# Kernel tuning notes

Measured on AMD Instinct MI355X. Metric: run time of the kernel, lower is better.

## Reference

```python
import jax, jax.numpy as jnp
import numpy as np

CUTOFFS = [0, 19997, 39997, 199997, 267735]  # cutoff_ends
SIZES = [19997, 20000, 160000, 67738]
DEMBS = [1024, 256, 64, 16]  # d_embed // div_val**i, div_val=4
N, D_PROJ = 1024, 1024


def setup_inputs() -> dict:
    key = jax.random.key(0)
    ks = jax.random.split(key, 20)
    inp = {
        "hidden": jax.random.normal(ks[0], (N, D_PROJ), jnp.float32),
        "target": jax.random.randint(ks[1], (N,), 0, CUTOFFS[-1], dtype=jnp.int64),
    }
    for i in range(4):
        inp[f"W{i}"] = 0.02 * jax.random.normal(ks[2 + 3 * i], (SIZES[i], DEMBS[i]), jnp.float32)
        inp[f"b{i}"] = jnp.zeros((SIZES[i],), jnp.float32)
        inp[f"p{i}"] = 0.02 * jax.random.normal(ks[3 + 3 * i], (D_PROJ, DEMBS[i]), jnp.float32)
    inp["cluster_weight"] = 0.02 * jax.random.normal(ks[14], (3, DEMBS[0]), jnp.float32)
    inp["cluster_bias"] = jnp.zeros((3,), jnp.float32)
    return inp


def _logit(hidden, W, b, p):
    # einsum('bd,de,ev->bv', hidden, proj, weight.T) + bias
    return (hidden @ p) @ W.T + b


def reference(hidden, target, W0, b0, p0, W1, b1, p1, W2, b2, p2, W3, b3, p3,
              cluster_weight, cluster_bias):
    n = hidden.shape[0]
    rows = jnp.arange(n)
    shortlist = W0.shape[0]  # 19997

    # head cluster: shortlist vocab + 3 cluster logits
    head_w = jnp.concatenate([W0, cluster_weight], axis=0)   # [shortlist+3, d_embed]
    head_b = jnp.concatenate([b0, cluster_bias], axis=0)
    head_lp = jax.nn.log_softmax(_logit(hidden, head_w, head_b, p0), axis=-1)  # [N, shortlist+3]

    masks = [target < CUTOFFS[1]]
    lps = [head_lp[rows, jnp.clip(target, 0, shortlist - 1)]]

    for i, (W, b, p) in enumerate([(W1, b1, p1), (W2, b2, p2), (W3, b3, p3)], start=1):
        l_idx, r_idx = CUTOFFS[i], CUTOFFS[i + 1]
        tail_lp = jax.nn.log_softmax(_logit(hidden, W, b, p), axis=-1)  # [N, r-l]
        rel = jnp.clip(target - l_idx, 0, r_idx - l_idx - 1)
        lps.append(head_lp[:, shortlist + i - 1] + tail_lp[rows, rel])
        masks.append((target >= l_idx) & (target < r_idx))

    logprob = jnp.select(masks, lps)
    return -logprob  # nll, shape [N]
```

## Files before the change

### kernel.cpp

```cpp
#include <hip/hip_runtime.h>
#include <stdint.h>

typedef short v8s __attribute__((ext_vector_type(8)));
typedef float f4 __attribute__((ext_vector_type(4)));
typedef unsigned short u16;
typedef unsigned int u32;

#define CUT1 19997
#define CUT2 39997
#define CUT3 199997
#define NROWS 1024
#define LDP 1360

#define NG_HEAD 157
#define NG_T1 40
#define NG_T2 157
#define NG_T3 67

__device__ __forceinline__ u32 pack2(float a, float b) {
    return (__float_as_uint(a) >> 16) | (__float_as_uint(b) & 0xffff0000u);
}
__device__ __forceinline__ float b2f(u16 h) { return __uint_as_float(((u32)h) << 16); }
__device__ __forceinline__ u16 f2b(float f) { return (u16)(__float_as_uint(f) >> 16); }

__device__ __forceinline__ void gload16(const void* g, void* l) {
    __builtin_amdgcn_global_load_lds(
        (const __attribute__((address_space(1))) u32*)g,
        (__attribute__((address_space(3))) u32*)l, 16, 0, 0);
}

__device__ __forceinline__ void cast8(const float* __restrict__ in, u16* __restrict__ out, size_t j) {
    const float4* p = (const float4*)(in + j * 8);
    float4 a = p[0], b = p[1];
    uint4 o = { pack2(a.x, a.y), pack2(a.z, a.w), pack2(b.x, b.y), pack2(b.z, b.w) };
    *(uint4*)(out + j * 8) = o;
}

__global__ __launch_bounds__(256) void prep_small_k(
    const float* __restrict__ hidden,
    const float* __restrict__ p0, const float* __restrict__ p1,
    const float* __restrict__ p2, const float* __restrict__ p3,
    const int* __restrict__ target,
    u16* __restrict__ hb, u16* __restrict__ pTb,
    int* __restrict__ cnt, int* __restrict__ slot,
    int* __restrict__ rowmap)
{
    int bid = blockIdx.x;
    int tid = threadIdx.x;

    if (bid < 512) {
        cast8(hidden, hb, bid * 256 + tid);
        return;
    }
    if (bid < 1888) {
        int b = bid - 512;
        const float* src; int d, rowOff, bx, by;
        if (b < 1024)      { src = p0; d = 1024; rowOff = 0;    bx = b & 31;          by = b >> 5; }
        else if (b < 1280) { src = p1; d = 256;  rowOff = 1024; bx = (b - 1024) & 7;  by = (b - 1024) >> 3; }
        else if (b < 1344) { src = p2; d = 64;   rowOff = 1280; bx = (b - 1280) & 1;  by = (b - 1280) >> 1; }
        else               { src = p3; d = 16;   rowOff = 1344; bx = 0;               by = b - 1344; }
        __shared__ float tile[32][33];
        int tx = tid & 31, ty = tid >> 5;
        int x = bx * 32 + tx;
        int ybase = by * 32;
#pragma unroll
        for (int j = 0; j < 4; ++j) {
            int r = ty + j * 8;
            tile[r][tx] = (x < d) ? src[(size_t)(ybase + r) * d + x] : 0.f;
        }
        __syncthreads();
#pragma unroll
        for (int j = 0; j < 4; ++j) {
            int x2 = bx * 32 + ty + j * 8;
            if (x2 < d) pTb[(size_t)(rowOff + x2) * 1024 + ybase + tx] = f2b(tile[tx][ty + j * 8]);
        }
        return;
    }

    __shared__ int lcnt[3];
    for (int i = tid; i < 3072; i += 256) rowmap[i] = 0;
    if (tid < 3) lcnt[tid] = 0;
    __syncthreads();
    for (int r = tid; r < NROWS; r += 256) {
        int t = target[r];
        int c = (t < CUT1) ? -1 : (t < CUT2) ? 0 : (t < CUT3) ? 1 : 2;
        int s = -1;
        if (c >= 0) {
            s = atomicAdd(&lcnt[c], 1);
            rowmap[c * 1024 + s] = r;
        }
        slot[r] = s;
    }
    __syncthreads();
    if (tid < 3) cnt[tid] = lcnt[tid];
}

template<int MODE, int NCOL>
__device__ __forceinline__ void gemm_body(
    u16* __restrict__ As, u16* __restrict__ Bs,
    const u16* __restrict__ A, int lda, const int* __restrict__ rowmap,
    const u16* __restrict__ B, int ldb,
    const float* __restrict__ bias, int N, int K,
    u16* __restrict__ Cout, int ldc,
    float* __restrict__ pout, const int* __restrict__ count,
    int bx, int byg)
{
    const int tid = threadIdx.x;
    const int rbase = bx * 128;
    if (MODE == 1 && count) {
        int c = *count;
        if (rbase >= ((c + 127) & ~127)) return;
    }

    const int wave = tid >> 6, lane = tid & 63;
    const int l4 = lane & 15, quad = lane >> 4;
    const int wg = (wave >> 1) * 4;
    const int cg = (wave & 1) * 4;

    const int g0 = tid >> 6, seg0 = (tid >> 4) & 3, r0 = tid & 15;
    const int s1 = 256 + tid;
    const int g1 = s1 >> 6, seg1 = (s1 >> 4) & 3, r1 = s1 & 15;

    const u16 *Asrc0, *Asrc1;
    {
        int ar0 = rbase + g0 * 16 + r0, ar1 = rbase + g1 * 16 + r1;
        if (rowmap) { ar0 = rowmap[ar0]; ar1 = rowmap[ar1]; }
        Asrc0 = A + (size_t)ar0 * lda + seg0 * 8;
        Asrc1 = A + (size_t)ar1 * lda + seg1 * 8;
    }
    u16* Ad0 = &As[tid * 8]; u16* Ad1 = &As[(256 + tid) * 8];
    u16* Bd0 = &Bs[tid * 8]; u16* Bd1 = &Bs[(256 + tid) * 8];

    float part[4][4];
    if (MODE == 1) {
#pragma unroll
        for (int r = 0; r < 4; ++r)
#pragma unroll
            for (int g = 0; g < 4; ++g) part[r][g] = 0.f;
    }

    const int wr = wg * 16, wc = cg * 16;

    for (int ct = 0; ct < NCOL; ++ct) {
        const int cbase = (byg * NCOL + ct) * 128;
        int bc0 = cbase + g0 * 16 + r0; if (bc0 >= N) bc0 = N - 1;
        int bc1 = cbase + g1 * 16 + r1; if (bc1 >= N) bc1 = N - 1;
        const u16* Bsrc0 = B + (size_t)bc0 * ldb + seg0 * 8;
        const u16* Bsrc1 = B + (size_t)bc1 * ldb + seg1 * 8;

        f4 acc[4][4] = {};
        for (int kk = 0; kk < K; kk += 32) {
            gload16(Asrc0 + kk, Ad0);
            gload16(Asrc1 + kk, Ad1);
            gload16(Bsrc0 + kk, Bd0);
            gload16(Bsrc1 + kk, Bd1);
            __syncthreads();
            v8s af[4], bf[4];
#pragma unroll
            for (int r = 0; r < 4; ++r)
                af[r] = *(const v8s*)&As[((wg + r) * 64 + quad * 16 + l4) * 8];
#pragma unroll
            for (int c = 0; c < 4; ++c)
                bf[c] = *(const v8s*)&Bs[((cg + c) * 64 + quad * 16 + l4) * 8];
#pragma unroll
            for (int r = 0; r < 4; ++r)
#pragma unroll
                for (int c = 0; c < 4; ++c)
                    acc[r][c] = __builtin_amdgcn_mfma_f32_16x16x32_bf16(af[r], bf[c], acc[r][c], 0, 0, 0);
            __syncthreads();
        }

        if (MODE == 0) {
#pragma unroll
            for (int c = 0; c < 4; ++c) {
                int col = cbase + wc + c * 16 + l4;
                if (col < N) {
#pragma unroll
                    for (int r = 0; r < 4; ++r)
#pragma unroll
                        for (int g = 0; g < 4; ++g) {
                            int row = rbase + wr + r * 16 + quad * 4 + g;
                            Cout[(size_t)row * ldc + col] = f2b(acc[r][c][g]);
                        }
                }
            }
        } else {
#pragma unroll
            for (int c = 0; c < 4; ++c) {
                int col = cbase + wc + c * 16 + l4;
                if (col < N) {
                    float bb = bias[col];
#pragma unroll
                    for (int r = 0; r < 4; ++r)
#pragma unroll
                        for (int g = 0; g < 4; ++g)
                            part[r][g] += __expf(acc[r][c][g] + bb);
                }
            }
        }
    }

    if (MODE == 1) {
#pragma unroll
        for (int off = 1; off < 16; off <<= 1)
#pragma unroll
            for (int r = 0; r < 4; ++r)
#pragma unroll
                for (int g = 0; g < 4; ++g)
                    part[r][g] += __shfl_xor(part[r][g], off);
        float v = part[0][0];
#pragma unroll
        for (int r = 0; r < 4; ++r)
#pragma unroll
            for (int g = 0; g < 4; ++g)
                if (l4 == r * 4 + g) v = part[r][g];
        int rowoff = (l4 >> 2) * 16 + quad * 4 + (l4 & 3);
        float* lbuf = (float*)As;
        lbuf[(wave & 1) * 128 + wr + rowoff] = v;
        __syncthreads();
        if (tid < 128) pout[rbase + tid] = lbuf[tid] + lbuf[128 + tid];
    }
}

#define CP_E0 2559616
#define CP_E1 3199616
#define CP_E2 4479616
__global__ __launch_bounds__(256) void castproj_k(
    const u16* __restrict__ hb, const u16* __restrict__ pTb, u16* __restrict__ proj,
    const float* __restrict__ W0, const float* __restrict__ W1,
    const float* __restrict__ W2, const float* __restrict__ W3,
    u16* __restrict__ W0b, u16* __restrict__ W1b,
    u16* __restrict__ W2b, u16* __restrict__ W3b)
{
    __shared__ __align__(16) u16 As[4096];
    __shared__ __align__(16) u16 Bs[4096];
    int bid = blockIdx.x;
    if (bid < 88) {
        gemm_body<0, 1>(As, Bs, hb, 1024, nullptr, pTb, 1024, nullptr, 1360, 1024,
                        proj, LDP, nullptr, nullptr, bid & 7, bid >> 3);
        return;
    }
    int i = (bid - 88) * 256 + threadIdx.x;
    if (i < CP_E0) { cast8(W0, W0b, i); return; }
    if (i < CP_E1) { cast8(W1, W1b, i - CP_E0); return; }
    if (i < CP_E2) { cast8(W2, W2b, i - CP_E1); return; }
    int r = i - CP_E2;
    if (r >= 67738) return;
    const float4* p = (const float4*)(W3 + (size_t)r * 16);
    float4 a = p[0], b = p[1], c = p[2], d = p[3];
    uint4 o0 = { pack2(a.x, a.y), pack2(a.z, a.w), pack2(b.x, b.y), pack2(b.z, b.w) };
    uint4 o1 = { pack2(c.x, c.y), pack2(c.z, c.w), pack2(d.x, d.y), pack2(d.z, d.w) };
    uint4 z = { 0, 0, 0, 0 };
    uint4* q = (uint4*)(W3b + (size_t)r * 32);
    q[0] = o0; q[1] = o1; q[2] = z; q[3] = z;
}

#define SE_GRID 3368
__global__ __launch_bounds__(256) void sumexp_k(
    const u16* __restrict__ proj,
    const u16* __restrict__ W0b, const u16* __restrict__ W1b,
    const u16* __restrict__ W2b, const u16* __restrict__ W3b,
    const float* __restrict__ b0, const float* __restrict__ b1,
    const float* __restrict__ b2, const float* __restrict__ b3,
    float* __restrict__ Ph, float* __restrict__ Pt1,
    float* __restrict__ Pt2, float* __restrict__ Pt3,
    const int* __restrict__ rmap, const int* __restrict__ cnt)
{
    __shared__ __align__(16) u16 As[4096];
    __shared__ __align__(16) u16 Bs[4096];
    int bid = blockIdx.x;
    if (bid < 1256) {
        gemm_body<1, 1>(As, Bs, proj, LDP, nullptr, W0b, 1024, b0, CUT1, 1024,
                        nullptr, 0, Ph + (size_t)(bid >> 3) * 1024, nullptr, bid & 7, bid >> 3);
    } else if (bid < 1576) {
        int rel = bid - 1256;
        gemm_body<1, 4>(As, Bs, proj + 1024, LDP, rmap, W1b, 256, b1, 20000, 256,
                        nullptr, 0, Pt1 + (size_t)(rel >> 3) * 1024, cnt + 0, rel & 7, rel >> 3);
    } else if (bid < 2832) {
        int rel = bid - 1576;
        gemm_body<1, 8>(As, Bs, proj + 1280, LDP, rmap + 1024, W2b, 64, b2, 160000, 64,
                        nullptr, 0, Pt2 + (size_t)(rel >> 3) * 1024, cnt + 1, rel & 7, rel >> 3);
    } else {
        int rel = bid - 2832;
        gemm_body<1, 8>(As, Bs, proj + 1344, LDP, rmap + 2048, W3b, 32, b3, 67738, 32,
                        nullptr, 0, Pt3 + (size_t)(rel >> 3) * 1024, cnt + 2, rel & 7, rel >> 3);
    }
}

__global__ __launch_bounds__(256) void final_k(
    const u16* __restrict__ proj, const int* __restrict__ target, const int* __restrict__ slot,
    const float* __restrict__ cw, const float* __restrict__ cb,
    const float* __restrict__ W0, const float* __restrict__ b0,
    const float* __restrict__ W1, const float* __restrict__ b1,
    const float* __restrict__ W2, const float* __restrict__ b2,
    const float* __restrict__ W3, const float* __restrict__ b3,
    const float* __restrict__ Ph, const float* __restrict__ Pt1,
    const float* __restrict__ Pt2, const float* __restrict__ Pt3,
    float* __restrict__ out)
{
    int row = blockIdx.x * 4 + (threadIdx.x >> 6);
    int lane = threadIdx.x & 63;
    const u16* pr = proj + (size_t)row * LDP;

    float c0 = 0.f, c1 = 0.f, c2 = 0.f;
    for (int k = lane; k < 1024; k += 64) {
        float pv = b2f(pr[k]);
        c0 += pv * cw[k]; c1 += pv * cw[1024 + k]; c2 += pv * cw[2048 + k];
    }
    float hs = 0.f;
    for (int g = lane; g < NG_HEAD; g += 64) hs += Ph[g * 1024 + row];

    int t = target[row];
    const float* W; const float* bb; int K, off, rel;
    const float* Pc = Ph; int gc = 0;
    if (t < CUT1)      { W = W0; bb = b0; K = 1024; off = 0;    rel = t; }
    else if (t < CUT2) { W = W1; bb = b1; K = 256;  off = 1024; rel = t - CUT1; Pc = Pt1; gc = NG_T1; }
    else if (t < CUT3) { W = W2; bb = b2; K = 64;   off = 1280; rel = t - CUT2; Pc = Pt2; gc = NG_T2; }
    else               { W = W3; bb = b3; K = 16;   off = 1344; rel = t - CUT3; Pc = Pt3; gc = NG_T3; }

    float ts = 0.f;
    int s = slot[row];
    if (s >= 0) {
        for (int g = lane; g < gc; g += 64) ts += Pc[g * 1024 + s];
    }
    float acc = 0.f;
    const float* wr = W + (size_t)rel * K;
    for (int k = lane; k < K; k += 64) acc += b2f(pr[off + k]) * wr[k];

#pragma unroll
    for (int o2 = 1; o2 < 64; o2 <<= 1) {
        c0 += __shfl_xor(c0, o2); c1 += __shfl_xor(c1, o2); c2 += __shfl_xor(c2, o2);
        hs += __shfl_xor(hs, o2); ts += __shfl_xor(ts, o2); acc += __shfl_xor(acc, o2);
    }

    if (lane == 0) {
        c0 += cb[0]; c1 += cb[1]; c2 += cb[2];
        float tl = acc + bb[rel];
        float lseh = __logf(hs + __expf(c0) + __expf(c1) + __expf(c2));
        float lp;
        if (t < CUT1) lp = tl - lseh;
        else {
            int c = (t < CUT2) ? 0 : (t < CUT3) ? 1 : 2;
            float cc = (c == 0) ? c0 : (c == 1) ? c1 : c2;
            lp = (cc - lseh) + (tl - __logf(ts));
        }
        out[row] = -lp;
    }
}

__global__ void cast_bf16_k(const float* __restrict__ in, u16* __restrict__ out, int n8) {
    int i = blockIdx.x * 256 + threadIdx.x;
    if (i >= n8) return;
    cast8(in, out, i);
}

__global__ void transpose_f_k(const float* __restrict__ in, float* __restrict__ out, int d, int rowOff) {
    __shared__ float tile[32][33];
    int tx = threadIdx.x, ty = threadIdx.y;
    int x = blockIdx.x * 32 + tx;
    int ybase = blockIdx.y * 32;
#pragma unroll
    for (int j = 0; j < 4; ++j) {
        int r = ty + j * 8;
        tile[r][tx] = (x < d) ? in[(size_t)(ybase + r) * d + x] : 0.f;
    }
    __syncthreads();
#pragma unroll
    for (int j = 0; j < 4; ++j) {
        int x2 = blockIdx.x * 32 + ty + j * 8;
        if (x2 < d) out[(size_t)(rowOff + x2) * 1024 + ybase + tx] = tile[tx][ty + j * 8];
    }
}

__global__ __launch_bounds__(256) void gemm_tn_k(
    const u16* __restrict__ A, int lda,
    const float* __restrict__ B, int ldb,
    const float* __restrict__ bias, int N, int K,
    u16* __restrict__ Cout, int ldc, float* __restrict__ rowsum)
{
    int tid = threadIdx.x;
    int wave = tid >> 6, lane = tid & 63;
    int l4 = lane & 15, quad = lane >> 4;
    int rbase = blockIdx.x * 16;
    int cbase = blockIdx.y * 256 + wave * 64;

    f4 acc[4] = {};
    v8s zero8 = {0, 0, 0, 0, 0, 0, 0, 0};
    const u16* arow = A + (size_t)(rbase + l4) * lda;
    int nk = (K + 31) >> 5;
    for (int kt = 0; kt < nk; ++kt) {
        int kk = (kt << 5) + quad * 8;
        v8s a = (kk < K) ? *(const v8s*)(arow + kk) : zero8;
#pragma unroll
        for (int t = 0; t < 4; ++t) {
            int col = cbase + t * 16 + l4;
            v8s b = zero8;
            if ((col < N) && (kk < K)) {
                const float* bp = B + (size_t)col * ldb + kk;
                float4 f0 = *(const float4*)bp;
                float4 f1 = *(const float4*)(bp + 4);
                union { uint4 u; v8s s; } bu;
                bu.u.x = pack2(f0.x, f0.y); bu.u.y = pack2(f0.z, f0.w);
                bu.u.z = pack2(f1.x, f1.y); bu.u.w = pack2(f1.z, f1.w);
                b = bu.s;
            }
            acc[t] = __builtin_amdgcn_mfma_f32_16x16x32_bf16(a, b, acc[t], 0, 0, 0);
        }
    }
    if (Cout) {
#pragma unroll
        for (int t = 0; t < 4; ++t) {
            int col = cbase + t * 16 + l4;
            if (col < N) {
#pragma unroll
                for (int r = 0; r < 4; ++r)
                    Cout[(size_t)(rbase + quad * 4 + r) * ldc + col] = f2b(acc[t][r]);
            }
        }
    } else {
        float part[4] = {0.f, 0.f, 0.f, 0.f};
#pragma unroll
        for (int t = 0; t < 4; ++t) {
            int col = cbase + t * 16 + l4;
            if (col < N) {
                float bb = bias[col];
#pragma unroll
                for (int r = 0; r < 4; ++r) part[r] += __expf(acc[t][r] + bb);
            }
        }
#pragma unroll
        for (int off = 1; off < 16; off <<= 1)
#pragma unroll
            for (int r = 0; r < 4; ++r) part[r] += __shfl_xor(part[r], off);
        if (l4 < 4) {
            float v = (l4 == 0) ? part[0] : (l4 == 1) ? part[1] : (l4 == 2) ? part[2] : part[3];
            atomicAdd(&rowsum[rbase + quad * 4 + l4], v);
        }
    }
}

__global__ __launch_bounds__(256) void gather_k(
    const u16* __restrict__ proj, const int* __restrict__ target,
    const float* __restrict__ cw, const float* __restrict__ cb,
    const float* __restrict__ W0, const float* __restrict__ b0,
    const float* __restrict__ W1, const float* __restrict__ b1,
    const float* __restrict__ W2, const float* __restrict__ b2,
    const float* __restrict__ W3, const float* __restrict__ b3,
    float* __restrict__ rs_head, float* __restrict__ cl, float* __restrict__ tl)
{
    int row = blockIdx.x * 4 + (threadIdx.x >> 6);
    int lane = threadIdx.x & 63;
    const u16* pr = proj + (size_t)row * LDP;

    float c0 = 0.f, c1 = 0.f, c2 = 0.f;
    for (int k = lane; k < 1024; k += 64) {
        float pv = b2f(pr[k]);
        c0 += pv * cw[k]; c1 += pv * cw[1024 + k]; c2 += pv * cw[2048 + k];
    }
#pragma unroll
    for (int off = 1; off < 64; off <<= 1) {
        c0 += __shfl_xor(c0, off); c1 += __shfl_xor(c1, off); c2 += __shfl_xor(c2, off);
    }
    int t = target[row];
    const float* W; const float* bb; int K, off, rel;
    if (t < CUT1)      { W = W0; bb = b0; K = 1024; off = 0;    rel = t; }
    else if (t < CUT2) { W = W1; bb = b1; K = 256;  off = 1024; rel = t - CUT1; }
    else if (t < CUT3) { W = W2; bb = b2; K = 64;   off = 1280; rel = t - CUT2; }
    else               { W = W3; bb = b3; K = 16;   off = 1344; rel = t - CUT3; }
    float acc = 0.f;
    const float* wr = W + (size_t)rel * K;
    for (int k = lane; k < K; k += 64) acc += b2f(pr[off + k]) * wr[k];
#pragma unroll
    for (int o2 = 1; o2 < 64; o2 <<= 1) acc += __shfl_xor(acc, o2);
    if (lane == 0) {
        c0 += cb[0]; c1 += cb[1]; c2 += cb[2];
        cl[row * 3 + 0] = c0; cl[row * 3 + 1] = c1; cl[row * 3 + 2] = c2;
        atomicAdd(&rs_head[row], __expf(c0) + __expf(c1) + __expf(c2));
        tl[row] = acc + bb[rel];
    }
}

__global__ void finalize_full_k(const int* __restrict__ target, const float* __restrict__ rs,
                                const float* __restrict__ cl, const float* __restrict__ tl,
                                float* __restrict__ out)
{
    int i = blockIdx.x * 256 + threadIdx.x;
    if (i >= NROWS) return;
    int t = target[i];
    float lseh = __logf(rs[i]);
    float lp;
    if (t < CUT1) lp = tl[i] - lseh;
    else {
        int c = (t < CUT2) ? 0 : (t < CUT3) ? 1 : 2;
        lp = (cl[i * 3 + c] - lseh) + (tl[i] - __logf(rs[(c + 1) * 1024 + i]));
    }
    out[i] = -lp;
}

extern "C" void kernel_launch(void* const* d_in, const int* in_sizes, int n_in,
                              void* d_out, int out_size, void* d_ws, size_t ws_size,
                              hipStream_t stream)
{
    const float* hidden = (const float*)d_in[0];
    const int*   target = (const int*)d_in[1];
    const float* W0 = (const float*)d_in[2];
    const float* b0 = (const float*)d_in[3];
    const float* p0 = (const float*)d_in[4];
    const float* W1 = (const float*)d_in[5];
    const float* b1 = (const float*)d_in[6];
    const float* p1 = (const float*)d_in[7];
    const float* W2 = (const float*)d_in[8];
    const float* b2 = (const float*)d_in[9];
    const float* p2 = (const float*)d_in[10];
    const float* W3 = (const float*)d_in[11];
    const float* b3 = (const float*)d_in[12];
    const float* p3 = (const float*)d_in[13];
    const float* cw = (const float*)d_in[14];
    const float* cb = (const float*)d_in[15];
    float* out = (float*)d_out;
    char* w = (char*)d_ws;

    if (ws_size >= 84000000ull) {
        u16*   hb   = (u16*)(w + 0);
        u16*   pTb  = (u16*)(w + 2097152);
        float* Ph   = (float*)(w + 0);
        float* Pt1  = (float*)(w + 643072);
        float* Pt2  = (float*)(w + 806912);
        float* Pt3  = (float*)(w + 1449984);
        u16*   proj = (u16*)(w + 4882432);
        u16*   W0b  = (u16*)(w + 7667712);
        u16*   W1b  = (u16*)(w + 48621568);
        u16*   W2b  = (u16*)(w + 58861568);
        u16*   W3b  = (u16*)(w + 79341568);
        int*   cnt  = (int*)(w + 83693184);
        int*   slot = (int*)(w + 83693200);
        int*   rmap = (int*)(w + 83697296);

        prep_small_k<<<1889, 256, 0, stream>>>(hidden, p0, p1, p2, p3, target,
                                               hb, pTb, cnt, slot, rmap);

        castproj_k<<<17852, 256, 0, stream>>>(hb, pTb, proj,
                                              W0, W1, W2, W3, W0b, W1b, W2b, W3b);

        sumexp_k<<<SE_GRID, 256, 0, stream>>>(proj, W0b, W1b, W2b, W3b,
                                              b0, b1, b2, b3,
                                              Ph, Pt1, Pt2, Pt3, rmap, cnt);

        final_k<<<256, 256, 0, stream>>>(proj, target, slot, cw, cb,
                                         W0, b0, W1, b1, W2, b2, W3, b3,
                                         Ph, Pt1, Pt2, Pt3, out);
    } else {
        float* pT   = (float*)w;
        u16*   hb   = (u16*)(w + 5570560);
        u16*   proj = (u16*)(w + 7667712);
        float* rs   = (float*)(w + 10452992);
        float* cl   = (float*)(w + 10469376);
        float* tl   = (float*)(w + 10481664);
        dim3 tb(32, 8);

        hipMemsetAsync(rs, 0, 4 * 1024 * sizeof(float), stream);
        cast_bf16_k<<<512, 256, 0, stream>>>(hidden, hb, 131072);
        transpose_f_k<<<dim3(32, 32), tb, 0, stream>>>(p0, pT, 1024, 0);
        transpose_f_k<<<dim3(8, 32),  tb, 0, stream>>>(p1, pT, 256, 1024);
        transpose_f_k<<<dim3(2, 32),  tb, 0, stream>>>(p2, pT, 64, 1280);
        transpose_f_k<<<dim3(1, 32),  tb, 0, stream>>>(p3, pT, 16, 1344);

        gemm_tn_k<<<dim3(64, 6), 256, 0, stream>>>(hb, 1024, pT, 1024, nullptr,
                                                   1360, 1024, proj, LDP, nullptr);
        gemm_tn_k<<<dim3(64, 79), 256, 0, stream>>>(proj, LDP, W0, 1024, b0,
                                                    CUT1, 1024, nullptr, 0, rs);
        gemm_tn_k<<<dim3(64, 79), 256, 0, stream>>>(proj + 1024, LDP, W1, 256, b1,
                                                    20000, 256, nullptr, 0, rs + 1024);
        gemm_tn_k<<<dim3(64, 625), 256, 0, stream>>>(proj + 1280, LDP, W2, 64, b2,
                                                     160000, 64, nullptr, 0, rs + 2048);
        gemm_tn_k<<<dim3(64, 265), 256, 0, stream>>>(proj + 1344, LDP, W3, 16, b3,
                                                     67738, 16, nullptr, 0, rs + 3072);

        gather_k<<<256, 256, 0, stream>>>(proj, target, cw, cb,
                                          W0, b0, W1, b1, W2, b2, W3, b3, rs, cl, tl);
        finalize_full_k<<<4, 256, 0, stream>>>(target, rs, cl, tl, out);
    }
}
```

Measured before the change: 430.8 us.

## Triple-buffer GEMM loads with async pipeline, remap blocks for XCD locality

The shared GEMM body now uses a three-stage LDS ring. Global-to-LDS loads run two steps ahead, with explicit vmcnt waits and one barrier per step in place of two. The K-loop and column-tile loop are flattened into one fully unrolled compile-time loop, and MFMA issue priority is raised. Block indices are remapped so consecutive blocks, which are spread across XCDs, cover contiguous column groups, bias is staged in LDS, and launch bounds request three blocks per CU. This triples LDS use per block and adds padding blocks that exit early.

```diff
diff --git a/kernel.cpp b/kernel.cpp
--- a/kernel.cpp
+++ b/kernel.cpp
@@ -95,31 +95,34 @@
     if (tid < 3) cnt[tid] = lcnt[tid];
 }
 
-template<int MODE, int NCOL>
+template<int MODE, int NCOL, int K>
 __device__ __forceinline__ void gemm_body(
-    u16* __restrict__ As, u16* __restrict__ Bs,
+    u16* __restrict__ As, u16* __restrict__ Bs, float* __restrict__ bsm,
     const u16* __restrict__ A, int lda, const int* __restrict__ rowmap,
     const u16* __restrict__ B, int ldb,
-    const float* __restrict__ bias, int N, int K,
+    const float* __restrict__ bias, int N,
     u16* __restrict__ Cout, int ldc,
     float* __restrict__ pout, const int* __restrict__ count,
     int bx, int byg)
 {
+    constexpr int nk = K / 32;
+    constexpr int total = NCOL * nk;
+
     const int tid = threadIdx.x;
     const int rbase = bx * 128;
     if (MODE == 1 && count) {
         int c = *count;
         if (rbase >= ((c + 127) & ~127)) return;
     }
-
     const int wave = tid >> 6, lane = tid & 63;
     const int l4 = lane & 15, quad = lane >> 4;
     const int wg = (wave >> 1) * 4;
     const int cg = (wave & 1) * 4;
+    const int wr = wg * 16, wc = cg * 16;
 
     const int g0 = tid >> 6, seg0 = (tid >> 4) & 3, r0 = tid & 15;
-    const int s1 = 256 + tid;
-    const int g1 = s1 >> 6, seg1 = (s1 >> 4) & 3, r1 = s1 & 15;
+    const int s1i = 256 + tid;
+    const int g1 = s1i >> 6, seg1 = (s1i >> 4) & 3, r1 = s1i & 15;
 
     const u16 *Asrc0, *Asrc1;
     {
@@ -128,8 +131,30 @@
         Asrc0 = A + (size_t)ar0 * lda + seg0 * 8;
         Asrc1 = A + (size_t)ar1 * lda + seg1 * 8;
     }
-    u16* Ad0 = &As[tid * 8]; u16* Ad1 = &As[(256 + tid) * 8];
-    u16* Bd0 = &Bs[tid * 8]; u16* Bd1 = &Bs[(256 + tid) * 8];
+
+    if (MODE == 1) {
+        const int cb0 = byg * (NCOL * 128);
+        for (int i2 = tid; i2 < NCOL * 128; i2 += 256) {
+            int col = cb0 + i2;
+            bsm[i2] = (col < N) ? bias[col] : 0.f;
+        }
+        __syncthreads();
+    }
+
+    auto stage = [&](int s2) {
+        const int buf = s2 % 3;
+        const int kk = (s2 % nk) * 32;
+        const int ct = s2 / nk;
+        const int cb = (byg * NCOL + ct) * 128;
+        int bc0 = cb + g0 * 16 + r0; if (bc0 >= N) bc0 = N - 1;
+        int bc1 = cb + g1 * 16 + r1; if (bc1 >= N) bc1 = N - 1;
+        u16* bA = As + buf * 4096;
+        u16* bB = Bs + buf * 4096;
+        gload16(Asrc0 + kk, bA + tid * 8);
+        gload16(Asrc1 + kk, bA + (256 + tid) * 8);
+        gload16(B + (size_t)bc0 * ldb + seg0 * 8 + kk, bB + tid * 8);
+        gload16(B + (size_t)bc1 * ldb + seg1 * 8 + kk, bB + (256 + tid) * 8);
+    };
 
     float part[4][4];
     if (MODE == 1) {
@@ -139,62 +164,77 @@
             for (int g = 0; g < 4; ++g) part[r][g] = 0.f;
     }
 
-    const int wr = wg * 16, wc = cg * 16;
-
-    for (int ct = 0; ct < NCOL; ++ct) {
-        const int cbase = (byg * NCOL + ct) * 128;
-        int bc0 = cbase + g0 * 16 + r0; if (bc0 >= N) bc0 = N - 1;
-        int bc1 = cbase + g1 * 16 + r1; if (bc1 >= N) bc1 = N - 1;
-        const u16* Bsrc0 = B + (size_t)bc0 * ldb + seg0 * 8;
-        const u16* Bsrc1 = B + (size_t)bc1 * ldb + seg1 * 8;
-
-        f4 acc[4][4] = {};
-        for (int kk = 0; kk < K; kk += 32) {
-            gload16(Asrc0 + kk, Ad0);
-            gload16(Asrc1 + kk, Ad1);
-            gload16(Bsrc0 + kk, Bd0);
-            gload16(Bsrc1 + kk, Bd1);
-            __syncthreads();
-            v8s af[4], bf[4];
+    stage(0);
+    if (total > 1) stage(1);
+
+    const f4 zero4 = {0.f, 0.f, 0.f, 0.f};
+    f4 acc[4][4];
+
+#pragma unroll
+    for (int s = 0; s < total; ++s) {
+        if (s + 1 < total) asm volatile("s_waitcnt vmcnt(4)" ::: "memory");
+        else               asm volatile("s_waitcnt vmcnt(0)" ::: "memory");
+        __builtin_amdgcn_sched_barrier(0);
+        __builtin_amdgcn_s_barrier();
+        __builtin_amdgcn_sched_barrier(0);
+
+        const int buf = s % 3;
+        const u16* Ab = As + buf * 4096;
+        const u16* Bb = Bs + buf * 4096;
+        v8s af[4], bf[4];
+#pragma unroll
+        for (int r = 0; r < 4; ++r)
+            af[r] = *(const v8s*)&Ab[((wg + r) * 64 + quad * 16 + l4) * 8];
+#pragma unroll
+        for (int c = 0; c < 4; ++c)
+            bf[c] = *(const v8s*)&Bb[((cg + c) * 64 + quad * 16 + l4) * 8];
+
+        if (s + 2 < total) stage(s + 2);
+
+        if ((s % nk) == 0) {
 #pragma unroll
             for (int r = 0; r < 4; ++r)
-                af[r] = *(const v8s*)&As[((wg + r) * 64 + quad * 16 + l4) * 8];
+#pragma unroll
+                for (int c = 0; c < 4; ++c) acc[r][c] = zero4;
+        }
+
+        __builtin_amdgcn_s_setprio(1);
+#pragma unroll
+        for (int r = 0; r < 4; ++r)
 #pragma unroll
             for (int c = 0; c < 4; ++c)
-                bf[c] = *(const v8s*)&Bs[((cg + c) * 64 + quad * 16 + l4) * 8];
-#pragma unroll
-            for (int r = 0; r < 4; ++r)
-#pragma unroll
-                for (int c = 0; c < 4; ++c)
-                    acc[r][c] = __builtin_amdgcn_mfma_f32_16x16x32_bf16(af[r], bf[c], acc[r][c], 0, 0, 0);
-            __syncthreads();
-        }
-
-        if (MODE == 0) {
-#pragma unroll
-            for (int c = 0; c < 4; ++c) {
-                int col = cbase + wc + c * 16 + l4;
-                if (col < N) {
-#pragma unroll
-                    for (int r = 0; r < 4; ++r)
-#pragma unroll
-                        for (int g = 0; g < 4; ++g) {
-                            int row = rbase + wr + r * 16 + quad * 4 + g;
-                            Cout[(size_t)row * ldc + col] = f2b(acc[r][c][g]);
-                        }
+                acc[r][c] = __builtin_amdgcn_mfma_f32_16x16x32_bf16(af[r], bf[c], acc[r][c], 0, 0, 0);
+        __builtin_amdgcn_s_setprio(0);
+
+        if ((s % nk) == nk - 1) {
+            const int ct = s / nk;
+            const int cbase = (byg * NCOL + ct) * 128;
+            if (MODE == 0) {
+#pragma unroll
+                for (int c = 0; c < 4; ++c) {
+                    int col = cbase + wc + c * 16 + l4;
+                    if (col < N) {
+#pragma unroll
+                        for (int r = 0; r < 4; ++r)
+#pragma unroll
+                            for (int g = 0; g < 4; ++g) {
+                                int row = rbase + wr + r * 16 + quad * 4 + g;
+                                Cout[(size_t)row * ldc + col] = f2b(acc[r][c][g]);
+                            }
+                    }
                 }
-            }
-        } else {
-#pragma unroll
-            for (int c = 0; c < 4; ++c) {
-                int col = cbase + wc + c * 16 + l4;
-                if (col < N) {
-                    float bb = bias[col];
-#pragma unroll
-                    for (int r = 0; r < 4; ++r)
-#pragma unroll
-                        for (int g = 0; g < 4; ++g)
-                            part[r][g] += __expf(acc[r][c][g] + bb);
+            } else {
+#pragma unroll
+                for (int c = 0; c < 4; ++c) {
+                    int col = cbase + wc + c * 16 + l4;
+                    if (col < N) {
+                        float bb = bsm[ct * 128 + wc + c * 16 + l4];
+#pragma unroll
+                        for (int r = 0; r < 4; ++r)
+#pragma unroll
+                            for (int g = 0; g < 4; ++g)
+                                part[r][g] += __expf(acc[r][c][g] + bb);
+                    }
                 }
             }
         }
@@ -216,6 +256,7 @@
                 if (l4 == r * 4 + g) v = part[r][g];
         int rowoff = (l4 >> 2) * 16 + quad * 4 + (l4 & 3);
         float* lbuf = (float*)As;
+        __syncthreads();
         lbuf[(wave & 1) * 128 + wr + rowoff] = v;
         __syncthreads();
         if (tid < 128) pout[rbase + tid] = lbuf[tid] + lbuf[128 + tid];
@@ -225,22 +266,25 @@
 #define CP_E0 2559616
 #define CP_E1 3199616
 #define CP_E2 4479616
-__global__ __launch_bounds__(256) void castproj_k(
+__global__ __launch_bounds__(256, 3) void castproj_k(
     const u16* __restrict__ hb, const u16* __restrict__ pTb, u16* __restrict__ proj,
     const float* __restrict__ W0, const float* __restrict__ W1,
     const float* __restrict__ W2, const float* __restrict__ W3,
     u16* __restrict__ W0b, u16* __restrict__ W1b,
     u16* __restrict__ W2b, u16* __restrict__ W3b)
 {
-    __shared__ __align__(16) u16 As[4096];
-    __shared__ __align__(16) u16 Bs[4096];
+    __shared__ __align__(16) u16 As[3 * 4096];
+    __shared__ __align__(16) u16 Bs[3 * 4096];
     int bid = blockIdx.x;
-    if (bid < 88) {
-        gemm_body<0, 1>(As, Bs, hb, 1024, nullptr, pTb, 1024, nullptr, 1360, 1024,
-                        proj, LDP, nullptr, nullptr, bid & 7, bid >> 3);
+    if (bid < 128) {
+        int x = bid & 7, j = bid >> 3;
+        int byg = x * 2 + (j >> 3), bx = j & 7;
+        if (byg >= 11) return;
+        gemm_body<0, 1, 1024>(As, Bs, nullptr, hb, 1024, nullptr, pTb, 1024, nullptr, 1360,
+                              proj, LDP, nullptr, nullptr, bx, byg);
         return;
     }
-    int i = (bid - 88) * 256 + threadIdx.x;
+    int i = (bid - 128) * 256 + threadIdx.x;
     if (i < CP_E0) { cast8(W0, W0b, i); return; }
     if (i < CP_E1) { cast8(W1, W1b, i - CP_E0); return; }
     if (i < CP_E2) { cast8(W2, W2b, i - CP_E1); return; }
@@ -255,8 +299,8 @@
     q[0] = o0; q[1] = o1; q[2] = z; q[3] = z;
 }
 
-#define SE_GRID 3368
-__global__ __launch_bounds__(256) void sumexp_k(
+#define SE_GRID 3456
+__global__ __launch_bounds__(256, 3) void sumexp_k(
     const u16* __restrict__ proj,
     const u16* __restrict__ W0b, const u16* __restrict__ W1b,
     const u16* __restrict__ W2b, const u16* __restrict__ W3b,
@@ -266,24 +310,36 @@
     float* __restrict__ Pt2, float* __restrict__ Pt3,
     const int* __restrict__ rmap, const int* __restrict__ cnt)
 {
-    __shared__ __align__(16) u16 As[4096];
-    __shared__ __align__(16) u16 Bs[4096];
+    __shared__ __align__(16) u16 As[3 * 4096];
+    __shared__ __align__(16) u16 Bs[3 * 4096];
+    __shared__ __align__(16) float bsm[1024];
     int bid = blockIdx.x;
-    if (bid < 1256) {
-        gemm_body<1, 1>(As, Bs, proj, LDP, nullptr, W0b, 1024, b0, CUT1, 1024,
-                        nullptr, 0, Ph + (size_t)(bid >> 3) * 1024, nullptr, bid & 7, bid >> 3);
-    } else if (bid < 1576) {
-        int rel = bid - 1256;
-        gemm_body<1, 4>(As, Bs, proj + 1024, LDP, rmap, W1b, 256, b1, 20000, 256,
-                        nullptr, 0, Pt1 + (size_t)(rel >> 3) * 1024, cnt + 0, rel & 7, rel >> 3);
-    } else if (bid < 2832) {
-        int rel = bid - 1576;
-        gemm_body<1, 8>(As, Bs, proj + 1280, LDP, rmap + 1024, W2b, 64, b2, 160000, 64,
-                        nullptr, 0, Pt2 + (size_t)(rel >> 3) * 1024, cnt + 1, rel & 7, rel >> 3);
+    if (bid < 1280) {
+        int x = bid & 7, j = bid >> 3;
+        int byg = x * 20 + (j >> 3), bx = j & 7;
+        if (byg >= NG_HEAD) return;
+        gemm_body<1, 1, 1024>(As, Bs, bsm, proj, LDP, nullptr, W0b, 1024, b0, CUT1,
+                              nullptr, 0, Ph + (size_t)byg * 1024, nullptr, bx, byg);
+    } else if (bid < 1600) {
+        int rel = bid - 1280;
+        int x = rel & 7, j = rel >> 3;
+        int byg = x * 5 + (j >> 3), bx = j & 7;
+        gemm_body<1, 4, 256>(As, Bs, bsm, proj + 1024, LDP, rmap, W1b, 256, b1, 20000,
+                             nullptr, 0, Pt1 + (size_t)byg * 1024, cnt + 0, bx, byg);
+    } else if (bid < 2880) {
+        int rel = bid - 1600;
+        int x = rel & 7, j = rel >> 3;
+        int byg = x * 20 + (j >> 3), bx = j & 7;
+        if (byg >= NG_T2) return;
+        gemm_body<1, 8, 64>(As, Bs, bsm, proj + 1280, LDP, rmap + 1024, W2b, 64, b2, 160000,
+                            nullptr, 0, Pt2 + (size_t)byg * 1024, cnt + 1, bx, byg);
     } else {
-        int rel = bid - 2832;
-        gemm_body<1, 8>(As, Bs, proj + 1344, LDP, rmap + 2048, W3b, 32, b3, 67738, 32,
-                        nullptr, 0, Pt3 + (size_t)(rel >> 3) * 1024, cnt + 2, rel & 7, rel >> 3);
+        int rel = bid - 2880;
+        int x = rel & 7, j = rel >> 3;
+        int byg = x * 9 + (j >> 3), bx = j & 7;
+        if (byg >= NG_T3) return;
+        gemm_body<1, 8, 32>(As, Bs, bsm, proj + 1344, LDP, rmap + 2048, W3b, 32, b3, 67738,
+                            nullptr, 0, Pt3 + (size_t)byg * 1024, cnt + 2, bx, byg);
     }
 }
 
@@ -539,7 +595,7 @@
         prep_small_k<<<1889, 256, 0, stream>>>(hidden, p0, p1, p2, p3, target,
                                                hb, pTb, cnt, slot, rmap);
 
-        castproj_k<<<17852, 256, 0, stream>>>(hb, pTb, proj,
+        castproj_k<<<17892, 256, 0, stream>>>(hb, pTb, proj,
                                               W0, W1, W2, W3, W0b, W1b, W2b, W3b);
 
         sumexp_k<<<SE_GRID, 256, 0, stream>>>(proj, W0b, W1b, W2b, W3b,
```

After: 356.8 us. 1.21x faster.
